# Kernel tuning notes

Hardware: AMD Instinct MI355X
Metric: run time of the kernel (lower is better)

## Reference

```python
import jax, jax.numpy as jnp
import numpy as np

EPS = 1e-8

def dice(x, alpha):
    # Dice activation (dim=3): per-channel BN (batch stats over B,L axes), then gating.
    m = jnp.mean(x, axis=(0, 1), keepdims=True)
    v = jnp.var(x, axis=(0, 1), keepdims=True)
    p = jax.nn.sigmoid((x - m) * jax.lax.rsqrt(v + EPS))
    return p * x + (1.0 - p) * alpha * x


def setup_inputs() -> dict:
    key = jax.random.key(0)
    ks = jax.random.split(key, 12)
    B, L, D = 2048, 200, 128
    H1, H2 = 128, 32
    query = jax.random.normal(ks[0], (B, D), dtype=jnp.float32)
    keys = jax.random.normal(ks[1], (B, L, D), dtype=jnp.float32)
    keys_len = jax.random.randint(ks[2], (B,), 0, L)
    s1 = 1.0 / np.sqrt(4 * D)
    s2 = 1.0 / np.sqrt(H1)
    s3 = 1.0 / np.sqrt(H2)
    W1 = jax.random.uniform(ks[3], (4 * D, H1), minval=-s1, maxval=s1, dtype=jnp.float32)
    b1 = jax.random.uniform(ks[4], (H1,), minval=-s1, maxval=s1, dtype=jnp.float32)
    alpha1 = jnp.zeros((H1,), dtype=jnp.float32)
    W2 = jax.random.uniform(ks[5], (H1, H2), minval=-s2, maxval=s2, dtype=jnp.float32)
    b2 = jax.random.uniform(ks[6], (H2,), minval=-s2, maxval=s2, dtype=jnp.float32)
    alpha2 = jnp.zeros((H2,), dtype=jnp.float32)
    Wd = jax.random.uniform(ks[7], (H2, 1), minval=-s3, maxval=s3, dtype=jnp.float32)
    bd = jax.random.uniform(ks[8], (1,), minval=-s3, maxval=s3, dtype=jnp.float32)
    return {"query": query, "keys": keys, "keys_len": keys_len,
            "W1": W1, "b1": b1, "alpha1": alpha1,
            "W2": W2, "b2": b2, "alpha2": alpha2,
            "Wd": Wd, "bd": bd}


def reference(query, keys, keys_len, W1, b1, alpha1, W2, b2, alpha2, Wd, bd):
    B, L, D = keys.shape
    q = jnp.broadcast_to(query[:, None, :], (B, L, D))
    # concat/diff/product features -> (B, L, 4D)
    x = jnp.concatenate([q, keys, q - keys, q * keys], axis=-1)
    h = dice(x @ W1 + b1, alpha1)
    h = dice(h @ W2 + b2, alpha2)
    score = (h @ Wd + bd)[..., 0]            # (B, L)
    mask = jnp.arange(L) < keys_len[:, None]  # (B, L)
    score = jnp.where(mask, score, 0.0)
    # weighted-sum pooling: (B, L) x (B, L, D) -> (B, D)
    return jnp.einsum('bl,bld->bd', score, keys)
```

## Files before the change

### kernel.cpp

```cpp
#include <hip/hip_runtime.h>
#include <hip/hip_bf16.h>
#include <stdint.h>

typedef __attribute__((ext_vector_type(8))) short bf16x8;
typedef __attribute__((ext_vector_type(4))) float f32x4;

#define B_SZ 2048
#define L_SZ 200
#define D_SZ 128
#define NROWS (B_SZ * L_SZ)
#define NTILES (NROWS / 16)

__device__ __forceinline__ short f2bf(float f) {
    union { float f; uint32_t u; } v; v.f = f;
    uint32_t u = v.u;
    u += 0x7FFFu + ((u >> 16) & 1u);
    return (short)(u >> 16);
}
__device__ __forceinline__ float bf2f(short s) {
    union { uint32_t u; float f; } v; v.u = ((uint32_t)(uint16_t)s) << 16;
    return v.f;
}
__device__ __forceinline__ float sigm(float x) {
    return 1.0f / (1.0f + __expf(-x));
}

__global__ void k0_prep(const float* __restrict__ W1, const float* __restrict__ W2,
                        float* __restrict__ Aprime, ushort* __restrict__ Wf,
                        ushort* __restrict__ W2f, float* __restrict__ stats)
{
    const int total = 16384 + 32768 + 4096 + 512;
    for (int i = blockIdx.x * blockDim.x + threadIdx.x; i < total; i += gridDim.x * blockDim.x) {
        if (i < 16384) {
            int r = i >> 7, c = i & 127;
            Aprime[i] = W1[r * 128 + c] + W1[(256 + r) * 128 + c];
        } else if (i < 16384 + 32768) {
            int f = i - 16384;
            int j = f & 7, l = (f >> 3) & 63, kt = (f >> 9) & 7, ct = f >> 12;
            int kk = kt * 32 + ((l >> 4) << 3) + j;
            int col = (ct << 4) + (l & 15);
            float v = (kk < 128) ? (W1[(128 + kk) * 128 + col] - W1[(256 + kk) * 128 + col])
                                 : W1[(384 + (kk - 128)) * 128 + col];
            Wf[f] = (ushort)f2bf(v);
        } else if (i < 16384 + 32768 + 4096) {
            int f = i - (16384 + 32768);
            int j = f & 7, l = (f >> 3) & 63, kt = (f >> 9) & 3, ct = f >> 11;
            int kk = kt * 32 + ((l >> 4) << 3) + j;
            int col = (ct << 4) + (l & 15);
            W2f[f] = (ushort)f2bf(W2[kk * 32 + col]);
        } else {
            stats[i - (16384 + 32768 + 4096)] = 0.0f;
        }
    }
}

__global__ void k1_qA(const float* __restrict__ q, const float* __restrict__ Aprime,
                      const float* __restrict__ b1, float* __restrict__ qA)
{
    __shared__ float qs[128];
    int b = blockIdx.x, c = threadIdx.x;
    qs[c] = q[b * 128 + c];
    __syncthreads();
    float acc = b1[c];
    #pragma unroll 8
    for (int r = 0; r < 128; ++r) acc += qs[r] * Aprime[r * 128 + c];
    qA[b * 128 + c] = acc;
}

__global__ void __launch_bounds__(64, 2) k2_main(
    const float* __restrict__ query, const float* __restrict__ keys,
    const float* __restrict__ qA, const ushort* __restrict__ Wf,
    ushort* __restrict__ z1, float* __restrict__ stats1)
{
    const int lane = threadIdx.x;
    const int half = blockIdx.x & 1;
    const int colbase = half * 64;
    const int r15 = lane & 15, g = lane >> 4;

    bf16x8 bfr[4][8];
    #pragma unroll
    for (int ctl = 0; ctl < 4; ++ctl)
        #pragma unroll
        for (int kt = 0; kt < 8; ++kt) {
            int ct = half * 4 + ctl;
            bfr[ctl][kt] = *(const bf16x8*)(Wf + ((size_t)(ct * 8 + kt) * 64 + lane) * 8);
        }

    float ssum[4] = {0, 0, 0, 0}, ssq[4] = {0, 0, 0, 0};

    for (int rt = (blockIdx.x >> 1); rt < NTILES; rt += (gridDim.x >> 1)) {
        int rowA = rt * 16 + r15;
        int bA = rowA / 200;
        const float* kp = keys + (size_t)rowA * 128 + g * 8;
        const float* qp = query + (size_t)bA * 128 + g * 8;

        f32x4 kv[4][2], qv[4][2];
        #pragma unroll
        for (int kt = 0; kt < 4; ++kt) {
            kv[kt][0] = *(const f32x4*)(kp + kt * 32);
            kv[kt][1] = *(const f32x4*)(kp + kt * 32 + 4);
            qv[kt][0] = *(const f32x4*)(qp + kt * 32);
            qv[kt][1] = *(const f32x4*)(qp + kt * 32 + 4);
        }
        bf16x8 afr[8];
        #pragma unroll
        for (int kt = 0; kt < 4; ++kt) {
            bf16x8 ak, ac;
            #pragma unroll
            for (int h = 0; h < 2; ++h)
                #pragma unroll
                for (int j = 0; j < 4; ++j) {
                    float kf = kv[kt][h][j];
                    float qf = qv[kt][h][j];
                    ak[h * 4 + j] = f2bf(kf);
                    ac[h * 4 + j] = f2bf(qf * kf);
                }
            afr[kt] = ak;
            afr[4 + kt] = ac;
        }
        f32x4 acc[4];
        #pragma unroll
        for (int ctl = 0; ctl < 4; ++ctl) {
            acc[ctl] = (f32x4){0, 0, 0, 0};
            #pragma unroll
            for (int kt = 0; kt < 8; ++kt)
                acc[ctl] = __builtin_amdgcn_mfma_f32_16x16x32_bf16(afr[kt], bfr[ctl][kt], acc[ctl], 0, 0, 0);
        }
        int rowC = rt * 16 + g * 4;
        #pragma unroll
        for (int j = 0; j < 4; ++j) {
            int row = rowC + j;
            int bC = row / 200;
            #pragma unroll
            for (int ctl = 0; ctl < 4; ++ctl) {
                int col = colbase + ctl * 16 + r15;
                float v = acc[ctl][j] + qA[bC * 128 + col];
                ssum[ctl] += v;
                ssq[ctl] += v * v;
                z1[(size_t)row * 128 + col] = (ushort)f2bf(v);
            }
        }
    }
    #pragma unroll
    for (int ctl = 0; ctl < 4; ++ctl) {
        float s = ssum[ctl], q2 = ssq[ctl];
        s += __shfl_xor(s, 16); s += __shfl_xor(s, 32);
        q2 += __shfl_xor(q2, 16); q2 += __shfl_xor(q2, 32);
        if (g == 0) {
            int col = colbase + ctl * 16 + r15;
            atomicAdd(&stats1[col], s);
            atomicAdd(&stats1[128 + col], q2);
        }
    }
}

__global__ void k_fin(const float* __restrict__ raw, float* __restrict__ fin, int nch)
{
    int c = threadIdx.x;
    if (c >= nch) return;
    float n = (float)NROWS;
    float m = raw[c] / n;
    float v = raw[nch + c] / n - m * m;
    float r = rsqrtf(v + 1e-8f);
    fin[c] = r;
    fin[nch + c] = -m * r;
}

__global__ void __launch_bounds__(64, 2) k4_z2(
    const ushort* __restrict__ z1, const ushort* __restrict__ W2f,
    const float* __restrict__ fin1, const float* __restrict__ alpha1,
    const float* __restrict__ b2, float* __restrict__ z2, float* __restrict__ stats2)
{
    const int lane = threadIdx.x, r15 = lane & 15, g = lane >> 4;
    bf16x8 bfr[2][4];
    #pragma unroll
    for (int ct = 0; ct < 2; ++ct)
        #pragma unroll
        for (int kt = 0; kt < 4; ++kt)
            bfr[ct][kt] = *(const bf16x8*)(W2f + ((size_t)(ct * 4 + kt) * 64 + lane) * 8);

    float rstd[4][8], bias0[4][8], alp[4][8];
    #pragma unroll
    for (int kt = 0; kt < 4; ++kt)
        #pragma unroll
        for (int j = 0; j < 8; ++j) {
            int c = kt * 32 + g * 8 + j;
            rstd[kt][j] = fin1[c];
            bias0[kt][j] = fin1[128 + c];
            alp[kt][j] = alpha1[c];
        }
    float b2v[2] = { b2[r15], b2[16 + r15] };
    float ssum[2] = {0, 0}, ssq[2] = {0, 0};

    for (int rt = blockIdx.x; rt < NTILES; rt += gridDim.x) {
        int rowA = rt * 16 + r15;
        bf16x8 afr[4];
        #pragma unroll
        for (int kt = 0; kt < 4; ++kt) {
            bf16x8 zv = *(const bf16x8*)(z1 + (size_t)rowA * 128 + kt * 32 + g * 8);
            bf16x8 hv;
            #pragma unroll
            for (int j = 0; j < 8; ++j) {
                float z = bf2f(zv[j]);
                float zh = z * rstd[kt][j] + bias0[kt][j];
                float p = sigm(zh);
                float t = p + (1.0f - p) * alp[kt][j];
                hv[j] = f2bf(z * t);
            }
            afr[kt] = hv;
        }
        f32x4 acc[2];
        #pragma unroll
        for (int ct = 0; ct < 2; ++ct) {
            acc[ct] = (f32x4){0, 0, 0, 0};
            #pragma unroll
            for (int kt = 0; kt < 4; ++kt)
                acc[ct] = __builtin_amdgcn_mfma_f32_16x16x32_bf16(afr[kt], bfr[ct][kt], acc[ct], 0, 0, 0);
        }
        int rowC = rt * 16 + g * 4;
        #pragma unroll
        for (int j = 0; j < 4; ++j) {
            int row = rowC + j;
            #pragma unroll
            for (int ct = 0; ct < 2; ++ct) {
                float v = acc[ct][j] + b2v[ct];
                ssum[ct] += v;
                ssq[ct] += v * v;
                z2[(size_t)row * 32 + ct * 16 + r15] = v;
            }
        }
    }
    #pragma unroll
    for (int ct = 0; ct < 2; ++ct) {
        float s = ssum[ct], q2 = ssq[ct];
        s += __shfl_xor(s, 16); s += __shfl_xor(s, 32);
        q2 += __shfl_xor(q2, 16); q2 += __shfl_xor(q2, 32);
        if (g == 0) {
            int col = ct * 16 + r15;
            atomicAdd(&stats2[col], s);
            atomicAdd(&stats2[32 + col], q2);
        }
    }
}

__global__ void __launch_bounds__(256) k6_score_pool(
    const float* __restrict__ z2, const float* __restrict__ keys,
    const int* __restrict__ keys_len, const float* __restrict__ fin2,
    const float* __restrict__ alpha2, const float* __restrict__ Wd,
    const float* __restrict__ bd, float* __restrict__ out)
{
    __shared__ float pp[129];
    __shared__ float sc[200];
    __shared__ float part[2][128];
    int b = blockIdx.x, t = threadIdx.x;
    if (t < 64) pp[t] = fin2[t];
    else if (t < 96) pp[t] = alpha2[t - 64];
    else if (t < 128) pp[t] = Wd[t - 96];
    else if (t == 128) pp[128] = bd[0];
    __syncthreads();

    int klen = keys_len[b];
    if (t < 200) {
        const float* zp = z2 + ((size_t)b * 200 + t) * 32;
        f32x4 zr[8];
        #pragma unroll
        for (int i = 0; i < 8; ++i) zr[i] = ((const f32x4*)zp)[i];
        float s = pp[128];
        #pragma unroll
        for (int c = 0; c < 32; ++c) {
            float z = zr[c >> 2][c & 3];
            float zh = z * pp[c] + pp[32 + c];
            float p = sigm(zh);
            float h = z * (p + (1.0f - p) * pp[64 + c]);
            s += h * pp[96 + c];
        }
        sc[t] = (t < klen) ? s : 0.0f;
    }
    __syncthreads();

    int c = t & 127, prt = t >> 7;
    const float* kp = keys + ((size_t)b * 200 + prt * 100) * 128 + c;
    float acc = 0.0f;
    #pragma unroll 4
    for (int l = 0; l < 100; ++l) acc += sc[prt * 100 + l] * kp[(size_t)l * 128];
    part[prt][c] = acc;
    __syncthreads();
    if (t < 128) out[(size_t)b * 128 + t] = part[0][t] + part[1][t];
}

extern "C" void kernel_launch(void* const* d_in, const int* in_sizes, int n_in,
                              void* d_out, int out_size, void* d_ws, size_t ws_size,
                              hipStream_t stream) {
    const float* query    = (const float*)d_in[0];
    const float* keys     = (const float*)d_in[1];
    const int*   keys_len = (const int*)d_in[2];
    const float* W1       = (const float*)d_in[3];
    const float* b1       = (const float*)d_in[4];
    const float* alpha1   = (const float*)d_in[5];
    const float* W2       = (const float*)d_in[6];
    const float* b2       = (const float*)d_in[7];
    const float* alpha2   = (const float*)d_in[8];
    const float* Wd       = (const float*)d_in[9];
    const float* bd       = (const float*)d_in[10];
    float* out = (float*)d_out;

    char* ws = (char*)d_ws;
    ushort* z1     = (ushort*)(ws);
    float*  z2     = (float*)(ws + 104857600);
    float*  qA     = (float*)(ws + 157286400);
    float*  Aprime = (float*)(ws + 158334976);
    ushort* Wf     = (ushort*)(ws + 158400512);
    ushort* W2f    = (ushort*)(ws + 158466048);
    float*  stats  = (float*)(ws + 158474240);
    float*  fin1   = (float*)(ws + 158476288);
    float*  fin2   = (float*)(ws + 158477312);

    k0_prep<<<128, 256, 0, stream>>>(W1, W2, Aprime, Wf, W2f, stats);
    k1_qA<<<B_SZ, 128, 0, stream>>>(query, Aprime, b1, qA);
    k2_main<<<2048, 64, 0, stream>>>(query, keys, qA, Wf, z1, stats);
    k_fin<<<1, 128, 0, stream>>>(stats, fin1, 128);
    k4_z2<<<1600, 64, 0, stream>>>(z1, W2f, fin1, alpha1, b2, z2, stats + 256);
    k_fin<<<1, 32, 0, stream>>>(stats + 256, fin2, 32);
    k6_score_pool<<<B_SZ, 256, 0, stream>>>(z2, keys, keys_len, fin2, alpha2, Wd, bd, out);
}
```

Measured before the change: 261.4 us.

## Fold per-batch query into layer-1 weights, halving MFMA K per batch

The main GEMM now runs one block per batch element. Each block builds a query-specific bf16 weight fragment (B + q*C) once, so the keys-only A operand has K=128 instead of 256 and the q*k product features are no longer formed. Layer 2 gets a larger grid, the bf16 conversion uses the native cast, and the pooling kernel skips masked rows past keys_len. The trade-offs are per-block weight construction from fp32 tables, padded last tiles (200 is not a multiple of 16), and a different bf16 rounding point for q*C.

```diff
diff --git a/kernel.cpp b/kernel.cpp
--- a/kernel.cpp
+++ b/kernel.cpp
@@ -12,10 +12,8 @@
 #define NTILES (NROWS / 16)
 
 __device__ __forceinline__ short f2bf(float f) {
-    union { float f; uint32_t u; } v; v.f = f;
-    uint32_t u = v.u;
-    u += 0x7FFFu + ((u >> 16) & 1u);
-    return (short)(u >> 16);
+    __bf16 h = (__bf16)f;
+    return __builtin_bit_cast(short, h);
 }
 __device__ __forceinline__ float bf2f(short s) {
     union { uint32_t u; float f; } v; v.u = ((uint32_t)(uint16_t)s) << 16;
@@ -26,30 +24,35 @@
 }
 
 __global__ void k0_prep(const float* __restrict__ W1, const float* __restrict__ W2,
-                        float* __restrict__ Aprime, ushort* __restrict__ Wf,
-                        ushort* __restrict__ W2f, float* __restrict__ stats)
-{
-    const int total = 16384 + 32768 + 4096 + 512;
+                        float* __restrict__ Aprime, float* __restrict__ Bf32,
+                        float* __restrict__ Cf32, ushort* __restrict__ W2f,
+                        float* __restrict__ stats)
+{
+    const int total = 16384 + 16384 + 16384 + 4096 + 512;
     for (int i = blockIdx.x * blockDim.x + threadIdx.x; i < total; i += gridDim.x * blockDim.x) {
         if (i < 16384) {
             int r = i >> 7, c = i & 127;
             Aprime[i] = W1[r * 128 + c] + W1[(256 + r) * 128 + c];
-        } else if (i < 16384 + 32768) {
-            int f = i - 16384;
-            int j = f & 7, l = (f >> 3) & 63, kt = (f >> 9) & 7, ct = f >> 12;
-            int kk = kt * 32 + ((l >> 4) << 3) + j;
+        } else if (i < 32768) {
+            int e = i - 16384;
+            int j = e & 7, l = (e >> 3) & 63, kt = (e >> 9) & 3, ct = e >> 11;
+            int k = kt * 32 + ((l >> 4) << 3) + j;
             int col = (ct << 4) + (l & 15);
-            float v = (kk < 128) ? (W1[(128 + kk) * 128 + col] - W1[(256 + kk) * 128 + col])
-                                 : W1[(384 + (kk - 128)) * 128 + col];
-            Wf[f] = (ushort)f2bf(v);
-        } else if (i < 16384 + 32768 + 4096) {
-            int f = i - (16384 + 32768);
+            Bf32[e] = W1[(128 + k) * 128 + col] - W1[(256 + k) * 128 + col];
+        } else if (i < 49152) {
+            int e = i - 32768;
+            int j = e & 7, l = (e >> 3) & 63, kt = (e >> 9) & 3, ct = e >> 11;
+            int k = kt * 32 + ((l >> 4) << 3) + j;
+            int col = (ct << 4) + (l & 15);
+            Cf32[e] = W1[(384 + k) * 128 + col];
+        } else if (i < 49152 + 4096) {
+            int f = i - 49152;
             int j = f & 7, l = (f >> 3) & 63, kt = (f >> 9) & 3, ct = f >> 11;
             int kk = kt * 32 + ((l >> 4) << 3) + j;
             int col = (ct << 4) + (l & 15);
             W2f[f] = (ushort)f2bf(W2[kk * 32 + col]);
         } else {
-            stats[i - (16384 + 32768 + 4096)] = 0.0f;
+            stats[i - (49152 + 4096)] = 0.0f;
         }
     }
 }
@@ -69,87 +72,99 @@
 
 __global__ void __launch_bounds__(64, 2) k2_main(
     const float* __restrict__ query, const float* __restrict__ keys,
-    const float* __restrict__ qA, const ushort* __restrict__ Wf,
-    ushort* __restrict__ z1, float* __restrict__ stats1)
+    const float* __restrict__ qA, const float* __restrict__ Bf32,
+    const float* __restrict__ Cf32, ushort* __restrict__ z1,
+    float* __restrict__ stats1)
 {
     const int lane = threadIdx.x;
-    const int half = blockIdx.x & 1;
-    const int colbase = half * 64;
+    const int b = blockIdx.x;
     const int r15 = lane & 15, g = lane >> 4;
 
-    bf16x8 bfr[4][8];
-    #pragma unroll
-    for (int ctl = 0; ctl < 4; ++ctl)
-        #pragma unroll
-        for (int kt = 0; kt < 8; ++kt) {
-            int ct = half * 4 + ctl;
-            bfr[ctl][kt] = *(const bf16x8*)(Wf + ((size_t)(ct * 8 + kt) * 64 + lane) * 8);
-        }
-
-    float ssum[4] = {0, 0, 0, 0}, ssq[4] = {0, 0, 0, 0};
-
-    for (int rt = (blockIdx.x >> 1); rt < NTILES; rt += (gridDim.x >> 1)) {
-        int rowA = rt * 16 + r15;
-        int bA = rowA / 200;
-        const float* kp = keys + (size_t)rowA * 128 + g * 8;
-        const float* qp = query + (size_t)bA * 128 + g * 8;
-
-        f32x4 kv[4][2], qv[4][2];
+    f32x4 qv[4][2];
+    #pragma unroll
+    for (int kt = 0; kt < 4; ++kt) {
+        const float* qp = query + (size_t)b * 128 + kt * 32 + g * 8;
+        qv[kt][0] = *(const f32x4*)(qp);
+        qv[kt][1] = *(const f32x4*)(qp + 4);
+    }
+
+    bf16x8 wb[8][4];
+    #pragma unroll
+    for (int ct = 0; ct < 8; ++ct)
         #pragma unroll
         for (int kt = 0; kt < 4; ++kt) {
-            kv[kt][0] = *(const f32x4*)(kp + kt * 32);
-            kv[kt][1] = *(const f32x4*)(kp + kt * 32 + 4);
-            qv[kt][0] = *(const f32x4*)(qp + kt * 32);
-            qv[kt][1] = *(const f32x4*)(qp + kt * 32 + 4);
-        }
-        bf16x8 afr[8];
+            const int fi = ((ct * 4 + kt) * 64 + lane) * 8;
+            f32x4 b0 = *(const f32x4*)(Bf32 + fi);
+            f32x4 b1v = *(const f32x4*)(Bf32 + fi + 4);
+            f32x4 c0 = *(const f32x4*)(Cf32 + fi);
+            f32x4 c1 = *(const f32x4*)(Cf32 + fi + 4);
+            bf16x8 w;
+            #pragma unroll
+            for (int j = 0; j < 4; ++j) {
+                w[j]     = f2bf(b0[j]  + qv[kt][0][j] * c0[j]);
+                w[4 + j] = f2bf(b1v[j] + qv[kt][1][j] * c1[j]);
+            }
+            wb[ct][kt] = w;
+        }
+
+    float qa[8];
+    #pragma unroll
+    for (int ct = 0; ct < 8; ++ct) qa[ct] = qA[(size_t)b * 128 + ct * 16 + r15];
+
+    float ssum[8] = {0,0,0,0,0,0,0,0}, ssq[8] = {0,0,0,0,0,0,0,0};
+
+    const float* kbase = keys + (size_t)b * L_SZ * 128;
+    ushort* zbase = z1 + (size_t)b * L_SZ * 128;
+
+    for (int t = 0; t < 13; ++t) {
+        const int row0 = t * 16;
+        const int lrowc = min(row0 + r15, L_SZ - 1);
+        const float* kp = kbase + (size_t)lrowc * 128 + g * 8;
+
+        bf16x8 afr[4];
         #pragma unroll
         for (int kt = 0; kt < 4; ++kt) {
-            bf16x8 ak, ac;
-            #pragma unroll
-            for (int h = 0; h < 2; ++h)
+            f32x4 k0 = *(const f32x4*)(kp + kt * 32);
+            f32x4 k1 = *(const f32x4*)(kp + kt * 32 + 4);
+            bf16x8 a;
+            #pragma unroll
+            for (int j = 0; j < 4; ++j) { a[j] = f2bf(k0[j]); a[4 + j] = f2bf(k1[j]); }
+            afr[kt] = a;
+        }
+
+        f32x4 acc[8];
+        #pragma unroll
+        for (int ct = 0; ct < 8; ++ct) {
+            acc[ct] = (f32x4){0, 0, 0, 0};
+            #pragma unroll
+            for (int kt = 0; kt < 4; ++kt)
+                acc[ct] = __builtin_amdgcn_mfma_f32_16x16x32_bf16(afr[kt], wb[ct][kt], acc[ct], 0, 0, 0);
+        }
+
+        const int rbase = row0 + g * 4;
+        #pragma unroll
+        for (int j = 0; j < 4; ++j) {
+            const int row = rbase + j;
+            if (row < L_SZ) {
                 #pragma unroll
-                for (int j = 0; j < 4; ++j) {
-                    float kf = kv[kt][h][j];
-                    float qf = qv[kt][h][j];
-                    ak[h * 4 + j] = f2bf(kf);
-                    ac[h * 4 + j] = f2bf(qf * kf);
+                for (int ct = 0; ct < 8; ++ct) {
+                    float v = acc[ct][j] + qa[ct];
+                    ssum[ct] += v;
+                    ssq[ct] += v * v;
+                    zbase[(size_t)row * 128 + ct * 16 + r15] = (ushort)f2bf(v);
                 }
-            afr[kt] = ak;
-            afr[4 + kt] = ac;
-        }
-        f32x4 acc[4];
-        #pragma unroll
-        for (int ctl = 0; ctl < 4; ++ctl) {
-            acc[ctl] = (f32x4){0, 0, 0, 0};
-            #pragma unroll
-            for (int kt = 0; kt < 8; ++kt)
-                acc[ctl] = __builtin_amdgcn_mfma_f32_16x16x32_bf16(afr[kt], bfr[ctl][kt], acc[ctl], 0, 0, 0);
-        }
-        int rowC = rt * 16 + g * 4;
-        #pragma unroll
-        for (int j = 0; j < 4; ++j) {
-            int row = rowC + j;
-            int bC = row / 200;
-            #pragma unroll
-            for (int ctl = 0; ctl < 4; ++ctl) {
-                int col = colbase + ctl * 16 + r15;
-                float v = acc[ctl][j] + qA[bC * 128 + col];
-                ssum[ctl] += v;
-                ssq[ctl] += v * v;
-                z1[(size_t)row * 128 + col] = (ushort)f2bf(v);
-            }
-        }
-    }
-    #pragma unroll
-    for (int ctl = 0; ctl < 4; ++ctl) {
-        float s = ssum[ctl], q2 = ssq[ctl];
+            }
+        }
+    }
+
+    #pragma unroll
+    for (int ct = 0; ct < 8; ++ct) {
+        float s = ssum[ct], q2 = ssq[ct];
         s += __shfl_xor(s, 16); s += __shfl_xor(s, 32);
         q2 += __shfl_xor(q2, 16); q2 += __shfl_xor(q2, 32);
         if (g == 0) {
-            int col = colbase + ctl * 16 + r15;
-            atomicAdd(&stats1[col], s);
-            atomicAdd(&stats1[128 + col], q2);
+            atomicAdd(&stats1[ct * 16 + r15], s);
+            atomicAdd(&stats1[128 + ct * 16 + r15], q2);
         }
     }
 }
@@ -261,28 +276,32 @@
 
     int klen = keys_len[b];
     if (t < 200) {
-        const float* zp = z2 + ((size_t)b * 200 + t) * 32;
-        f32x4 zr[8];
-        #pragma unroll
-        for (int i = 0; i < 8; ++i) zr[i] = ((const f32x4*)zp)[i];
-        float s = pp[128];
-        #pragma unroll
-        for (int c = 0; c < 32; ++c) {
-            float z = zr[c >> 2][c & 3];
-            float zh = z * pp[c] + pp[32 + c];
-            float p = sigm(zh);
-            float h = z * (p + (1.0f - p) * pp[64 + c]);
-            s += h * pp[96 + c];
-        }
-        sc[t] = (t < klen) ? s : 0.0f;
+        float s = 0.0f;
+        if (t < klen) {
+            const float* zp = z2 + ((size_t)b * 200 + t) * 32;
+            f32x4 zr[8];
+            #pragma unroll
+            for (int i = 0; i < 8; ++i) zr[i] = ((const f32x4*)zp)[i];
+            s = pp[128];
+            #pragma unroll
+            for (int c = 0; c < 32; ++c) {
+                float z = zr[c >> 2][c & 3];
+                float zh = z * pp[c] + pp[32 + c];
+                float p = sigm(zh);
+                float h = z * (p + (1.0f - p) * pp[64 + c]);
+                s += h * pp[96 + c];
+            }
+        }
+        sc[t] = s;
     }
     __syncthreads();
 
     int c = t & 127, prt = t >> 7;
+    int lim = min(100, klen - prt * 100);
     const float* kp = keys + ((size_t)b * 200 + prt * 100) * 128 + c;
     float acc = 0.0f;
     #pragma unroll 4
-    for (int l = 0; l < 100; ++l) acc += sc[prt * 100 + l] * kp[(size_t)l * 128];
+    for (int l = 0; l < lim; ++l) acc += sc[prt * 100 + l] * kp[(size_t)l * 128];
     part[prt][c] = acc;
     __syncthreads();
     if (t < 128) out[(size_t)b * 128 + t] = part[0][t] + part[1][t];
@@ -309,17 +328,18 @@
     float*  z2     = (float*)(ws + 104857600);
     float*  qA     = (float*)(ws + 157286400);
     float*  Aprime = (float*)(ws + 158334976);
-    ushort* Wf     = (ushort*)(ws + 158400512);
-    ushort* W2f    = (ushort*)(ws + 158466048);
-    float*  stats  = (float*)(ws + 158474240);
-    float*  fin1   = (float*)(ws + 158476288);
-    float*  fin2   = (float*)(ws + 158477312);
-
-    k0_prep<<<128, 256, 0, stream>>>(W1, W2, Aprime, Wf, W2f, stats);
+    float*  Bf32   = (float*)(ws + 158400512);
+    float*  Cf32   = (float*)(ws + 158466048);
+    ushort* W2f    = (ushort*)(ws + 158531584);
+    float*  stats  = (float*)(ws + 158539776);
+    float*  fin1   = (float*)(ws + 158541824);
+    float*  fin2   = (float*)(ws + 158542848);
+
+    k0_prep<<<128, 256, 0, stream>>>(W1, W2, Aprime, Bf32, Cf32, W2f, stats);
     k1_qA<<<B_SZ, 128, 0, stream>>>(query, Aprime, b1, qA);
-    k2_main<<<2048, 64, 0, stream>>>(query, keys, qA, Wf, z1, stats);
+    k2_main<<<B_SZ, 64, 0, stream>>>(query, keys, qA, Bf32, Cf32, z1, stats);
     k_fin<<<1, 128, 0, stream>>>(stats, fin1, 128);
-    k4_z2<<<1600, 64, 0, stream>>>(z1, W2f, fin1, alpha1, b2, z2, stats + 256);
+    k4_z2<<<4096, 64, 0, stream>>>(z1, W2f, fin1, alpha1, b2, z2, stats + 256);
     k_fin<<<1, 32, 0, stream>>>(stats + 256, fin2, 32);
     k6_score_pool<<<B_SZ, 256, 0, stream>>>(z2, keys, keys_len, fin2, alpha2, Wd, bd, out);
 }
```

Result: slower. 282.5 us (+8.1%).
